# Kernel tuning notes

Measured on AMD Instinct MI355X. Metric: run time of the kernel, lower is better.

## Reference

```python
import jax, jax.numpy as jnp
import numpy as np

B, T, DM, DQ, DA, F, K = 128, 1024, 512, 1024, 128, 32, 31


def setup_inputs() -> dict:
    key = jax.random.key(0)
    ks = jax.random.split(key, 9)
    state = jax.random.uniform(ks[1], (B, T), dtype=jnp.float32)
    state = state / jnp.sum(state, axis=-1, keepdims=True)  # alignment-like
    return {
        "query": jax.random.normal(ks[0], (B, DQ), dtype=jnp.float32),
        "state": state,
        "prev_max_alignments": jax.random.randint(ks[2], (B,), 0, T, dtype=jnp.int32),
        "memory": jax.random.normal(ks[3], (B, T, DM), dtype=jnp.float32),
        "Wq": jax.random.normal(ks[4], (DQ, DA), dtype=jnp.float32) * 0.02,
        "Wmem": jax.random.normal(ks[5], (DM, DA), dtype=jnp.float32) * 0.02,
        "conv_k": jax.random.normal(ks[6], (K, 1, F), dtype=jnp.float32) * 0.02,
        "Wloc": jax.random.normal(ks[7], (F, DA), dtype=jnp.float32) * 0.02,
        "v_w": jax.random.normal(ks[8], (DA,), dtype=jnp.float32) * 0.02,
        "v_b": jnp.zeros((), dtype=jnp.float32),
    }


def reference(query, state, prev_max_alignments, memory, Wq, Wmem, conv_k, Wloc, v_w, v_b):
    # processed query: [B, 1, DA]
    pq = (query @ Wq)[:, None, :]
    # location features: Conv1D 'same', no bias, over cumulative alignments [B, T, 1]
    f = jax.lax.conv_general_dilated(
        state[:, :, None], conv_k,
        window_strides=(1,), padding="SAME",
        dimension_numbers=("NWC", "WIO", "NWC"),
    )  # [B, T, F]
    loc = f @ Wloc                      # [B, T, DA]
    keys = memory @ Wmem                # [B, T, DA]
    # additive tanh score -> [B, T]
    energy = jnp.tanh(keys + pq + loc) @ v_w + v_b
    alignments = jax.nn.softmax(energy, axis=-1)
    new_state = alignments + state      # is_cumulate=True
    # context: [B, DM]
    context = jnp.einsum("bt,btd->bd", alignments, memory)
    return context, alignments, new_state
```

## Files before the change

kernel.cpp:

```cpp
#include <hip/hip_runtime.h>
#include <math.h>

#define B  128
#define T  1024
#define DM 512
#define DQ 1024
#define DA 128
#define F  32
#define KW 31

typedef short s16x8 __attribute__((ext_vector_type(8)));
typedef float f32x4 __attribute__((ext_vector_type(4)));
typedef unsigned int u32;
typedef u32 u32x4 __attribute__((ext_vector_type(4)));
typedef __attribute__((address_space(1))) const unsigned int gu32;
typedef __attribute__((address_space(3))) unsigned int lu32;

__device__ __forceinline__ unsigned short f2bf(float f) {
    u32 u = __builtin_bit_cast(u32, f);
    u32 r = u + 0x7FFFu + ((u >> 16) & 1u);
    return (unsigned short)(r >> 16);
}
__device__ __forceinline__ float bf2f(unsigned short h) {
    u32 u = ((u32)h) << 16;
    return __builtin_bit_cast(float, u);
}
__device__ __forceinline__ float fast_tanh(float x) {
    float ax = fabsf(x);
    float e = __expf(-2.0f * ax);
    float t = 1.0f - 2.0f * e / (1.0f + e);
    return copysignf(t, x);
}

__device__ __forceinline__ void trunc_split_pack(f32x4 a, f32x4 b, s16x8& hi, s16x8& lo) {
    u32x4 hw, lw;
    #pragma unroll
    for (int p = 0; p < 4; ++p) {
        float f0 = (p < 2) ? a[2 * p] : b[2 * p - 4];
        float f1 = (p < 2) ? a[2 * p + 1] : b[2 * p - 3];
        u32 u0 = __builtin_bit_cast(u32, f0);
        u32 u1 = __builtin_bit_cast(u32, f1);
        u32 t0 = u0 & 0xFFFF0000u;
        u32 t1 = u1 & 0xFFFF0000u;
        float l0 = f0 - __builtin_bit_cast(float, t0);
        float l1 = f1 - __builtin_bit_cast(float, t1);
        hw[p] = (u0 >> 16) | t1;
        lw[p] = (__builtin_bit_cast(u32, l0) >> 16) | (__builtin_bit_cast(u32, l1) & 0xFFFF0000u);
    }
    hi = __builtin_bit_cast(s16x8, hw);
    lo = __builtin_bit_cast(s16x8, lw);
}

__global__ __launch_bounds__(128) void prep_kernel(
        const float* __restrict__ query, const float* __restrict__ Wq,
        const float* __restrict__ Wmem, const float* __restrict__ conv_k,
        const float* __restrict__ Wloc,
        float* __restrict__ pqp, unsigned short* __restrict__ wsplit,
        unsigned short* __restrict__ CWt) {
    int a = threadIdx.x;
    int blk = blockIdx.x;
    if (blk < 8 * B) {
        int b = blk >> 3, q = blk & 7;
        const float* qp = query + b * DQ + q * 128;
        const float* wp = Wq + (size_t)(q * 128) * DA + a;
        float s = 0.f;
        #pragma unroll 4
        for (int i = 0; i < 128; ++i) s += qp[i] * wp[(size_t)i * DA];
        pqp[(q * B + b) * DA + a] = s;
    } else if (blk < 8 * B + DM) {
        int k = blk - 8 * B;
        unsigned short hi = f2bf(Wmem[k * DA + a]);
        int c = k >> 6;
        int es = (k & 63) ^ ((a & 7) << 3);
        wsplit[c * 8192 + a * 64 + es] = hi;
    } else {
        int k = blk - (8 * B + DM);
        float s = 0.f;
        if (k < KW) {
            #pragma unroll
            for (int f = 0; f < F; ++f) s += conv_k[k * F + f] * Wloc[f * DA + a];
        }
        CWt[a * 32 + k] = f2bf(s);
    }
}

__global__ __launch_bounds__(256, 3) void energy_mfma(
        const float* __restrict__ memory, const float* __restrict__ state,
        const float* __restrict__ pqp, const unsigned short* __restrict__ wsplit,
        const unsigned short* __restrict__ CWt, const float* __restrict__ v_w,
        const float* __restrict__ v_b, float* __restrict__ energy,
        float* __restrict__ pctx, float2* __restrict__ ms) {
    __shared__ unsigned short Wlds[8192];
    __shared__ unsigned short cwlds[4096];
    __shared__ float stl[160];
    __shared__ float pql[DA];
    __shared__ float vwl[DA];
    __shared__ float el[128];

    int tid = threadIdx.x;
    int w = tid >> 6, l = tid & 63, r = l & 15, g = l >> 4;
    int b  = blockIdx.x >> 3;
    int tile = blockIdx.x & 7;
    int t0 = tile << 7;

    for (int i = tid; i < 160; i += 256) {
        int t = t0 - 15 + i;
        stl[i] = (i < 159 && t >= 0 && t < T) ? state[b * T + t] : 0.f;
    }
    if (tid < DA) {
        float s = 0.f;
        #pragma unroll
        for (int q = 0; q < 8; ++q) s += pqp[(q * B + b) * DA + tid];
        pql[tid] = s;
        vwl[tid] = v_w[tid];
    }

    #pragma unroll
    for (int rd = 0; rd < 2; ++rd)
        __builtin_amdgcn_global_load_lds((gu32*)(CWt + rd * 2048 + tid * 8),
                                         (lu32*)(cwlds + (w << 9) + rd * 2048), 16, 0, 0);

    f32x4 acc0[8], acc1[8];
    #pragma unroll
    for (int nt = 0; nt < 8; ++nt) {
        acc0[nt] = (f32x4){0.f, 0.f, 0.f, 0.f};
        acc1[nt] = (f32x4){0.f, 0.f, 0.f, 0.f};
    }

    const int swz8 = (r & 7) << 3;
    const size_t arow = ((size_t)(b * T + t0 + w * 32 + r)) * DM;
    const float* Abase = memory + arow + g * 8;

    f32x4 rA[8], rAn[8];
    {
        const float* p = Abase;
        #pragma unroll
        for (int kk = 0; kk < 2; ++kk) {
            rA[kk * 4 + 0] = *(const f32x4*)(p + kk * 32);
            rA[kk * 4 + 1] = *(const f32x4*)(p + kk * 32 + 4);
            rA[kk * 4 + 2] = *(const f32x4*)(p + kk * 32 + 16 * DM);
            rA[kk * 4 + 3] = *(const f32x4*)(p + kk * 32 + 16 * DM + 4);
        }
    }

    for (int c = 0; c < 8; ++c) {
        __syncthreads();
        {
            const unsigned short* src = wsplit + (size_t)c * 8192 + tid * 8;
            #pragma unroll
            for (int rd = 0; rd < 4; ++rd)
                __builtin_amdgcn_global_load_lds((gu32*)(src + rd * 2048),
                                                 (lu32*)(Wlds + (w << 9) + rd * 2048),
                                                 16, 0, 0);
        }
        __syncthreads();

        if (c < 7) {
            const float* p = Abase + (c + 1) * 64;
            #pragma unroll
            for (int kk = 0; kk < 2; ++kk) {
                rAn[kk * 4 + 0] = *(const f32x4*)(p + kk * 32);
                rAn[kk * 4 + 1] = *(const f32x4*)(p + kk * 32 + 4);
                rAn[kk * 4 + 2] = *(const f32x4*)(p + kk * 32 + 16 * DM);
                rAn[kk * 4 + 3] = *(const f32x4*)(p + kk * 32 + 16 * DM + 4);
            }
        }

        #pragma unroll
        for (int kk = 0; kk < 2; ++kk) {
            s16x8 Ah0, Al0, Ah1, Al1;
            trunc_split_pack(rA[kk * 4 + 0], rA[kk * 4 + 1], Ah0, Al0);
            trunc_split_pack(rA[kk * 4 + 2], rA[kk * 4 + 3], Ah1, Al1);
            int off = (kk * 32 + g * 8) ^ swz8;
            #pragma unroll
            for (int nt = 0; nt < 8; ++nt) {
                const unsigned short* bp = Wlds + (nt * 16 + r) * 64 + off;
                s16x8 Bh = *(const s16x8*)bp;
                acc0[nt] = __builtin_amdgcn_mfma_f32_16x16x32_bf16(Ah0, Bh, acc0[nt], 0, 0, 0);
                acc0[nt] = __builtin_amdgcn_mfma_f32_16x16x32_bf16(Al0, Bh, acc0[nt], 0, 0, 0);
                acc1[nt] = __builtin_amdgcn_mfma_f32_16x16x32_bf16(Ah1, Bh, acc1[nt], 0, 0, 0);
                acc1[nt] = __builtin_amdgcn_mfma_f32_16x16x32_bf16(Al1, Bh, acc1[nt], 0, 0, 0);
            }
        }
        #pragma unroll
        for (int j = 0; j < 8; ++j) rA[j] = rAn[j];
    }

    s16x8 st0, st1;
    {
        int base0 = w * 32 + r + g * 8;
        #pragma unroll
        for (int j = 0; j < 8; ++j) {
            st0[j] = (short)f2bf(stl[base0 + j]);
            st1[j] = (short)f2bf(stl[base0 + 16 + j]);
        }
    }
    #pragma unroll
    for (int nt = 0; nt < 8; ++nt) {
        const unsigned short* cp = cwlds + (nt * 16 + r) * 32 + g * 8;
        s16x8 cw = *(const s16x8*)cp;
        acc0[nt] = __builtin_amdgcn_mfma_f32_16x16x32_bf16(st0, cw, acc0[nt], 0, 0, 0);
        acc1[nt] = __builtin_amdgcn_mfma_f32_16x16x32_bf16(st1, cw, acc1[nt], 0, 0, 0);
    }

    float vb = *v_b;
    #pragma unroll
    for (int sub = 0; sub < 2; ++sub) {
        #pragma unroll
        for (int reg = 0; reg < 4; ++reg) {
            float p = 0.f;
            #pragma unroll
            for (int nt = 0; nt < 8; ++nt) {
                int col = nt * 16 + r;
                float v = (sub == 0) ? acc0[nt][reg] : acc1[nt][reg];
                p += fast_tanh(v + pql[col]) * vwl[col];
            }
            p += __shfl_xor(p, 1, 16);
            p += __shfl_xor(p, 2, 16);
            p += __shfl_xor(p, 4, 16);
            p += __shfl_xor(p, 8, 16);
            if (r == 0) {
                int tl = w * 32 + sub * 16 + g * 4 + reg;
                energy[b * T + t0 + tl] = p + vb;
                el[tl] = p + vb;
            }
        }
    }
    __syncthreads();

    float m_w = -1e30f;
    #pragma unroll
    for (int t = 0; t < 32; ++t) m_w = fmaxf(m_w, el[w * 32 + t]);
    float s_w = 0.f;
    f32x4 c0 = (f32x4){0.f, 0.f, 0.f, 0.f};
    f32x4 c1 = (f32x4){0.f, 0.f, 0.f, 0.f};
    const float* mb = memory + ((size_t)(b * T + t0 + w * 32)) * DM + l * 8;
    #pragma unroll 4
    for (int t = 0; t < 32; ++t) {
        float pw = __expf(el[w * 32 + t] - m_w);
        s_w += pw;
        f32x4 v0 = *(const f32x4*)(mb + (size_t)t * DM);
        f32x4 v1 = *(const f32x4*)(mb + (size_t)t * DM + 4);
        c0 += pw * v0;
        c1 += pw * v1;
    }
    float* po = pctx + ((size_t)(tile * 4 + w) * B + b) * DM + l * 8;
    *(f32x4*)po = c0;
    *(f32x4*)(po + 4) = c1;
    if (l == 0) ms[(tile * 4 + w) * B + b] = make_float2(m_w, s_w);
}

__global__ __launch_bounds__(256) void finalize_kernel(
        const float* __restrict__ energy, const float* __restrict__ state,
        const float2* __restrict__ ms, const float* __restrict__ pctx,
        float* __restrict__ alignments, float* __restrict__ new_state,
        float* __restrict__ context) {
    int b = blockIdx.x, tid = threadIdx.x;
    float m = -1e30f;
    #pragma unroll
    for (int i = 0; i < 32; ++i) m = fmaxf(m, ms[i * B + b].x);
    float sc[32];
    float S = 0.f;
    #pragma unroll
    for (int i = 0; i < 32; ++i) {
        float2 v = ms[i * B + b];
        float e = __expf(v.x - m);
        sc[i] = e;
        S += e * v.y;
    }
    float invS = 1.0f / S;

    f32x4 ev = ((const f32x4*)(energy + b * T))[tid];
    f32x4 a4;
    a4[0] = __expf(ev[0] - m) * invS;
    a4[1] = __expf(ev[1] - m) * invS;
    a4[2] = __expf(ev[2] - m) * invS;
    a4[3] = __expf(ev[3] - m) * invS;
    ((f32x4*)(alignments + b * T))[tid] = a4;
    f32x4 st4 = ((const f32x4*)(state + b * T))[tid];
    ((f32x4*)(new_state + b * T))[tid] = a4 + st4;

    #pragma unroll
    for (int j = 0; j < 2; ++j) {
        int d = tid + j * 256;
        float c = 0.f;
        #pragma unroll 8
        for (int i = 0; i < 32; ++i)
            c += sc[i] * pctx[((size_t)i * B + b) * DM + d];
        context[b * DM + d] = c * invS;
    }
}

extern "C" void kernel_launch(void* const* d_in, const int* in_sizes, int n_in,
                              void* d_out, int out_size, void* d_ws, size_t ws_size,
                              hipStream_t stream) {
    const float* query  = (const float*)d_in[0];
    const float* state  = (const float*)d_in[1];
    const float* memory = (const float*)d_in[3];
    const float* Wq     = (const float*)d_in[4];
    const float* Wmem   = (const float*)d_in[5];
    const float* conv_k = (const float*)d_in[6];
    const float* Wloc   = (const float*)d_in[7];
    const float* v_w    = (const float*)d_in[8];
    const float* v_b    = (const float*)d_in[9];

    float* out        = (float*)d_out;
    float* context    = out;
    float* alignments = out + B * DM;
    float* new_state  = out + B * DM + B * T;

    char* ws = (char*)d_ws;
    float*          pqp     = (float*)ws;
    unsigned short* wsplit  = (unsigned short*)(ws + 524288);
    unsigned short* CWt     = (unsigned short*)(ws + 655360);
    float*          energy  = (float*)(ws + 663552);
    float*          pctx    = (float*)(ws + 1187840);
    float2*         ms      = (float2*)(ws + 1187840 + 8388608);

    prep_kernel<<<dim3(8 * B + DM + 32), 128, 0, stream>>>(query, Wq, Wmem, conv_k, Wloc, pqp, wsplit, CWt);
    energy_mfma<<<dim3(B * (T / 128)), 256, 0, stream>>>(memory, state, pqp, wsplit, CWt, v_w, v_b, energy, pctx, ms);
    finalize_kernel<<<dim3(B), 256, 0, stream>>>(energy, state, ms, pctx, alignments, new_state, context);
}
```

Measured before the change: 120.7 us.

## Stage memory tile in LDS for context reuse and halve time tile

The energy kernel now uses 64-row time tiles and copies each memory tile it loads into a swizzled 128KB LDS buffer, so the context accumulation reads from LDS instead of fetching the memory rows from global a second time. Wmem bf16 fragments and the conv-weight fragments are now loaded straight from global into registers, which removes the per-chunk LDS staging and its block barriers. The LDS footprint forces one block per CU, which cuts latency hiding for the memory stream. Twice as many partial-context slices go to finalize, which doubles the partial-context workspace it must reduce.

```diff
diff --git a/kernel.cpp b/kernel.cpp
--- a/kernel.cpp
+++ b/kernel.cpp
@@ -8,13 +8,12 @@
 #define DA 128
 #define F  32
 #define KW 31
+#define TILE 64
 
 typedef short s16x8 __attribute__((ext_vector_type(8)));
 typedef float f32x4 __attribute__((ext_vector_type(4)));
 typedef unsigned int u32;
 typedef u32 u32x4 __attribute__((ext_vector_type(4)));
-typedef __attribute__((address_space(1))) const unsigned int gu32;
-typedef __attribute__((address_space(3))) unsigned int lu32;
 
 __device__ __forceinline__ unsigned short f2bf(float f) {
     u32 u = __builtin_bit_cast(u32, f);
@@ -71,8 +70,7 @@
         int k = blk - 8 * B;
         unsigned short hi = f2bf(Wmem[k * DA + a]);
         int c = k >> 6;
-        int es = (k & 63) ^ ((a & 7) << 3);
-        wsplit[c * 8192 + a * 64 + es] = hi;
+        wsplit[c * 8192 + a * 64 + (k & 63)] = hi;
     } else {
         int k = blk - (8 * B + DM);
         float s = 0.f;
@@ -84,28 +82,27 @@
     }
 }
 
-__global__ __launch_bounds__(256, 3) void energy_mfma(
+__global__ __launch_bounds__(256, 1) void energy_mfma(
         const float* __restrict__ memory, const float* __restrict__ state,
         const float* __restrict__ pqp, const unsigned short* __restrict__ wsplit,
         const unsigned short* __restrict__ CWt, const float* __restrict__ v_w,
         const float* __restrict__ v_b, float* __restrict__ energy,
         float* __restrict__ pctx, float2* __restrict__ ms) {
-    __shared__ unsigned short Wlds[8192];
-    __shared__ unsigned short cwlds[4096];
-    __shared__ float stl[160];
+    __shared__ float Atile[TILE * 512];
+    __shared__ float stl[TILE + 32];
     __shared__ float pql[DA];
     __shared__ float vwl[DA];
-    __shared__ float el[128];
+    __shared__ float el[TILE];
 
     int tid = threadIdx.x;
     int w = tid >> 6, l = tid & 63, r = l & 15, g = l >> 4;
-    int b  = blockIdx.x >> 3;
-    int tile = blockIdx.x & 7;
-    int t0 = tile << 7;
-
-    for (int i = tid; i < 160; i += 256) {
+    int b    = blockIdx.x >> 4;
+    int tile = blockIdx.x & 15;
+    int t0   = tile << 6;
+
+    for (int i = tid; i < TILE + 30; i += 256) {
         int t = t0 - 15 + i;
-        stl[i] = (i < 159 && t >= 0 && t < T) ? state[b * T + t] : 0.f;
+        stl[i] = (t >= 0 && t < T) ? state[b * T + t] : 0.f;
     }
     if (tid < DA) {
         float s = 0.f;
@@ -114,140 +111,114 @@
         pql[tid] = s;
         vwl[tid] = v_w[tid];
     }
-
-    #pragma unroll
-    for (int rd = 0; rd < 2; ++rd)
-        __builtin_amdgcn_global_load_lds((gu32*)(CWt + rd * 2048 + tid * 8),
-                                         (lu32*)(cwlds + (w << 9) + rd * 2048), 16, 0, 0);
-
-    f32x4 acc0[8], acc1[8];
+    __syncthreads();
+
+    f32x4 acc0[8];
+    #pragma unroll
+    for (int nt = 0; nt < 8; ++nt) acc0[nt] = (f32x4){0.f, 0.f, 0.f, 0.f};
+
+    const int rowl = w * 16 + r;
+    const int sw = (r & 7) << 2;
+    const float* Ab = memory + ((size_t)(b * T + t0 + rowl)) * DM + g * 8;
+
+    f32x4 rA[4], rAn[4];
+    {
+        rA[0] = *(const f32x4*)(Ab);
+        rA[1] = *(const f32x4*)(Ab + 4);
+        rA[2] = *(const f32x4*)(Ab + 32);
+        rA[3] = *(const f32x4*)(Ab + 36);
+    }
+
+    for (int c = 0; c < 8; ++c) {
+        s16x8 Bv0[8], Bv1[8];
+        const unsigned short* Bc = wsplit + (size_t)c * 8192 + r * 64 + g * 8;
+        #pragma unroll
+        for (int nt = 0; nt < 8; ++nt) {
+            Bv0[nt] = *(const s16x8*)(Bc + nt * 1024);
+            Bv1[nt] = *(const s16x8*)(Bc + nt * 1024 + 32);
+        }
+        if (c < 7) {
+            const float* p = Ab + (c + 1) * 64;
+            rAn[0] = *(const f32x4*)(p);
+            rAn[1] = *(const f32x4*)(p + 4);
+            rAn[2] = *(const f32x4*)(p + 32);
+            rAn[3] = *(const f32x4*)(p + 36);
+        }
+        s16x8 Ah0, Al0, Ah1, Al1;
+        trunc_split_pack(rA[0], rA[1], Ah0, Al0);
+        trunc_split_pack(rA[2], rA[3], Ah1, Al1);
+        {
+            int fbase = rowl * 512 + c * 64;
+            *(f32x4*)&Atile[(fbase + g * 8)          ^ sw] = rA[0];
+            *(f32x4*)&Atile[(fbase + g * 8 + 4)      ^ sw] = rA[1];
+            *(f32x4*)&Atile[(fbase + 32 + g * 8)     ^ sw] = rA[2];
+            *(f32x4*)&Atile[(fbase + 32 + g * 8 + 4) ^ sw] = rA[3];
+        }
+        #pragma unroll
+        for (int nt = 0; nt < 8; ++nt) {
+            acc0[nt] = __builtin_amdgcn_mfma_f32_16x16x32_bf16(Ah0, Bv0[nt], acc0[nt], 0, 0, 0);
+            acc0[nt] = __builtin_amdgcn_mfma_f32_16x16x32_bf16(Al0, Bv0[nt], acc0[nt], 0, 0, 0);
+            acc0[nt] = __builtin_amdgcn_mfma_f32_16x16x32_bf16(Ah1, Bv1[nt], acc0[nt], 0, 0, 0);
+            acc0[nt] = __builtin_amdgcn_mfma_f32_16x16x32_bf16(Al1, Bv1[nt], acc0[nt], 0, 0, 0);
+        }
+        #pragma unroll
+        for (int j = 0; j < 4; ++j) rA[j] = rAn[j];
+    }
+
+    s16x8 st0;
+    {
+        int base0 = w * 16 + r + g * 8;
+        #pragma unroll
+        for (int j = 0; j < 8; ++j) st0[j] = (short)f2bf(stl[base0 + j]);
+    }
     #pragma unroll
     for (int nt = 0; nt < 8; ++nt) {
-        acc0[nt] = (f32x4){0.f, 0.f, 0.f, 0.f};
-        acc1[nt] = (f32x4){0.f, 0.f, 0.f, 0.f};
-    }
-
-    const int swz8 = (r & 7) << 3;
-    const size_t arow = ((size_t)(b * T + t0 + w * 32 + r)) * DM;
-    const float* Abase = memory + arow + g * 8;
-
-    f32x4 rA[8], rAn[8];
-    {
-        const float* p = Abase;
-        #pragma unroll
-        for (int kk = 0; kk < 2; ++kk) {
-            rA[kk * 4 + 0] = *(const f32x4*)(p + kk * 32);
-            rA[kk * 4 + 1] = *(const f32x4*)(p + kk * 32 + 4);
-            rA[kk * 4 + 2] = *(const f32x4*)(p + kk * 32 + 16 * DM);
-            rA[kk * 4 + 3] = *(const f32x4*)(p + kk * 32 + 16 * DM + 4);
-        }
-    }
-
-    for (int c = 0; c < 8; ++c) {
-        __syncthreads();
-        {
-            const unsigned short* src = wsplit + (size_t)c * 8192 + tid * 8;
-            #pragma unroll
-            for (int rd = 0; rd < 4; ++rd)
-                __builtin_amdgcn_global_load_lds((gu32*)(src + rd * 2048),
-                                                 (lu32*)(Wlds + (w << 9) + rd * 2048),
-                                                 16, 0, 0);
-        }
-        __syncthreads();
-
-        if (c < 7) {
-            const float* p = Abase + (c + 1) * 64;
-            #pragma unroll
-            for (int kk = 0; kk < 2; ++kk) {
-                rAn[kk * 4 + 0] = *(const f32x4*)(p + kk * 32);
-                rAn[kk * 4 + 1] = *(const f32x4*)(p + kk * 32 + 4);
-                rAn[kk * 4 + 2] = *(const f32x4*)(p + kk * 32 + 16 * DM);
-                rAn[kk * 4 + 3] = *(const f32x4*)(p + kk * 32 + 16 * DM + 4);
-            }
-        }
-
-        #pragma unroll
-        for (int kk = 0; kk < 2; ++kk) {
-            s16x8 Ah0, Al0, Ah1, Al1;
-            trunc_split_pack(rA[kk * 4 + 0], rA[kk * 4 + 1], Ah0, Al0);
-            trunc_split_pack(rA[kk * 4 + 2], rA[kk * 4 + 3], Ah1, Al1);
-            int off = (kk * 32 + g * 8) ^ swz8;
-            #pragma unroll
-            for (int nt = 0; nt < 8; ++nt) {
-                const unsigned short* bp = Wlds + (nt * 16 + r) * 64 + off;
-                s16x8 Bh = *(const s16x8*)bp;
-                acc0[nt] = __builtin_amdgcn_mfma_f32_16x16x32_bf16(Ah0, Bh, acc0[nt], 0, 0, 0);
-                acc0[nt] = __builtin_amdgcn_mfma_f32_16x16x32_bf16(Al0, Bh, acc0[nt], 0, 0, 0);
-                acc1[nt] = __builtin_amdgcn_mfma_f32_16x16x32_bf16(Ah1, Bh, acc1[nt], 0, 0, 0);
-                acc1[nt] = __builtin_amdgcn_mfma_f32_16x16x32_bf16(Al1, Bh, acc1[nt], 0, 0, 0);
-            }
-        }
-        #pragma unroll
-        for (int j = 0; j < 8; ++j) rA[j] = rAn[j];
-    }
-
-    s16x8 st0, st1;
-    {
-        int base0 = w * 32 + r + g * 8;
-        #pragma unroll
-        for (int j = 0; j < 8; ++j) {
-            st0[j] = (short)f2bf(stl[base0 + j]);
-            st1[j] = (short)f2bf(stl[base0 + 16 + j]);
-        }
-    }
-    #pragma unroll
-    for (int nt = 0; nt < 8; ++nt) {
-        const unsigned short* cp = cwlds + (nt * 16 + r) * 32 + g * 8;
-        s16x8 cw = *(const s16x8*)cp;
+        s16x8 cw = *(const s16x8*)(CWt + (nt * 16 + r) * 32 + g * 8);
         acc0[nt] = __builtin_amdgcn_mfma_f32_16x16x32_bf16(st0, cw, acc0[nt], 0, 0, 0);
-        acc1[nt] = __builtin_amdgcn_mfma_f32_16x16x32_bf16(st1, cw, acc1[nt], 0, 0, 0);
     }
 
     float vb = *v_b;
     #pragma unroll
-    for (int sub = 0; sub < 2; ++sub) {
-        #pragma unroll
-        for (int reg = 0; reg < 4; ++reg) {
-            float p = 0.f;
-            #pragma unroll
-            for (int nt = 0; nt < 8; ++nt) {
-                int col = nt * 16 + r;
-                float v = (sub == 0) ? acc0[nt][reg] : acc1[nt][reg];
-                p += fast_tanh(v + pql[col]) * vwl[col];
-            }
-            p += __shfl_xor(p, 1, 16);
-            p += __shfl_xor(p, 2, 16);
-            p += __shfl_xor(p, 4, 16);
-            p += __shfl_xor(p, 8, 16);
-            if (r == 0) {
-                int tl = w * 32 + sub * 16 + g * 4 + reg;
-                energy[b * T + t0 + tl] = p + vb;
-                el[tl] = p + vb;
-            }
-        }
-    }
-    __syncthreads();
+    for (int reg = 0; reg < 4; ++reg) {
+        float p = 0.f;
+        #pragma unroll
+        for (int nt = 0; nt < 8; ++nt) {
+            int col = nt * 16 + r;
+            p += fast_tanh(acc0[nt][reg] + pql[col]) * vwl[col];
+        }
+        p += __shfl_xor(p, 1, 16);
+        p += __shfl_xor(p, 2, 16);
+        p += __shfl_xor(p, 4, 16);
+        p += __shfl_xor(p, 8, 16);
+        if (r == 0) {
+            int m = w * 16 + g * 4 + reg;
+            energy[b * T + t0 + m] = p + vb;
+            el[m] = p + vb;
+        }
+    }
 
     float m_w = -1e30f;
     #pragma unroll
-    for (int t = 0; t < 32; ++t) m_w = fmaxf(m_w, el[w * 32 + t]);
+    for (int t = 0; t < 16; ++t) m_w = fmaxf(m_w, el[w * 16 + t]);
     float s_w = 0.f;
     f32x4 c0 = (f32x4){0.f, 0.f, 0.f, 0.f};
     f32x4 c1 = (f32x4){0.f, 0.f, 0.f, 0.f};
-    const float* mb = memory + ((size_t)(b * T + t0 + w * 32)) * DM + l * 8;
     #pragma unroll 4
-    for (int t = 0; t < 32; ++t) {
-        float pw = __expf(el[w * 32 + t] - m_w);
+    for (int t = 0; t < 16; ++t) {
+        float pw = __expf(el[w * 16 + t] - m_w);
         s_w += pw;
-        f32x4 v0 = *(const f32x4*)(mb + (size_t)t * DM);
-        f32x4 v1 = *(const f32x4*)(mb + (size_t)t * DM + 4);
+        int fr = (w * 16 + t) * 512 + l * 8;
+        int swt = (t & 7) << 2;
+        f32x4 v0 = *(const f32x4*)&Atile[(fr)     ^ swt];
+        f32x4 v1 = *(const f32x4*)&Atile[(fr + 4) ^ swt];
         c0 += pw * v0;
         c1 += pw * v1;
     }
-    float* po = pctx + ((size_t)(tile * 4 + w) * B + b) * DM + l * 8;
+    int id = tile * 4 + w;
+    float* po = pctx + ((size_t)id * B + b) * DM + l * 8;
     *(f32x4*)po = c0;
     *(f32x4*)(po + 4) = c1;
-    if (l == 0) ms[(tile * 4 + w) * B + b] = make_float2(m_w, s_w);
+    if (l == 0) ms[id * B + b] = make_float2(m_w, s_w);
 }
 
 __global__ __launch_bounds__(256) void finalize_kernel(
@@ -256,18 +227,16 @@
         float* __restrict__ alignments, float* __restrict__ new_state,
         float* __restrict__ context) {
     int b = blockIdx.x, tid = threadIdx.x;
+    __shared__ float scs[64];
     float m = -1e30f;
-    #pragma unroll
-    for (int i = 0; i < 32; ++i) m = fmaxf(m, ms[i * B + b].x);
-    float sc[32];
+    for (int i = 0; i < 64; ++i) m = fmaxf(m, ms[i * B + b].x);
     float S = 0.f;
-    #pragma unroll
-    for (int i = 0; i < 32; ++i) {
+    for (int i = 0; i < 64; ++i) {
         float2 v = ms[i * B + b];
-        float e = __expf(v.x - m);
-        sc[i] = e;
-        S += e * v.y;
-    }
+        S += __expf(v.x - m) * v.y;
+    }
+    if (tid < 64) scs[tid] = __expf(ms[tid * B + b].x - m);
+    __syncthreads();
     float invS = 1.0f / S;
 
     f32x4 ev = ((const f32x4*)(energy + b * T))[tid];
@@ -285,8 +254,8 @@
         int d = tid + j * 256;
         float c = 0.f;
         #pragma unroll 8
-        for (int i = 0; i < 32; ++i)
-            c += sc[i] * pctx[((size_t)i * B + b) * DM + d];
+        for (int i = 0; i < 64; ++i)
+            c += scs[i] * pctx[((size_t)i * B + b) * DM + d];
         context[b * DM + d] = c * invS;
     }
 }
@@ -315,9 +284,9 @@
     unsigned short* CWt     = (unsigned short*)(ws + 655360);
     float*          energy  = (float*)(ws + 663552);
     float*          pctx    = (float*)(ws + 1187840);
-    float2*         ms      = (float2*)(ws + 1187840 + 8388608);
+    float2*         ms      = (float2*)(ws + 1187840 + 16777216);
 
     prep_kernel<<<dim3(8 * B + DM + 32), 128, 0, stream>>>(query, Wq, Wmem, conv_k, Wloc, pqp, wsplit, CWt);
-    energy_mfma<<<dim3(B * (T / 128)), 256, 0, stream>>>(memory, state, pqp, wsplit, CWt, v_w, v_b, energy, pctx, ms);
+    energy_mfma<<<dim3(B * (T / TILE)), 256, 0, stream>>>(memory, state, pqp, wsplit, CWt, v_w, v_b, energy, pctx, ms);
     finalize_kernel<<<dim3(B), 256, 0, stream>>>(energy, state, ms, pctx, alignments, new_state, context);
 }
```

Result: slower. 244.1 us (+102.2%).
